# Kernel tuning notes

Measured on AMD Instinct MI355X. Metric: run time of the kernel, lower is better.

The kernel has to match this reference:

```python
import jax, jax.numpy as jnp
import numpy as np
from jax import lax

DIM = 128          # embedding dim
LG = 3             # layer_gnn
LC = 3             # layer_cnn
LO = 2             # layer_output
WIN = 11           # window -> conv kernel 23x23, padding 11 (SAME)
NF = 10000         # n_fingerprint
NW = 10000         # n_word
NA = 4096          # n_atoms
NWORDS = 16384     # protein length


def setup_inputs() -> dict:
    key = jax.random.key(0)
    ks = jax.random.split(key, 16)
    s = 1.0 / np.sqrt(DIM)
    s2 = 1.0 / np.sqrt(2 * DIM)
    K = 2 * WIN + 1
    return {
        "fingerprints": jax.random.randint(ks[0], (NA,), 0, NF),
        # sparse-ish binary adjacency like a molecular graph, scaled up
        "adjacency": (jax.random.uniform(ks[1], (NA, NA)) < 0.005).astype(jnp.float32),
        "words": jax.random.randint(ks[2], (NWORDS,), 0, NW),
        "emb_fp": jax.random.normal(ks[3], (NF, DIM), dtype=jnp.float32) * 0.1,
        "emb_word": jax.random.normal(ks[4], (NW, DIM), dtype=jnp.float32) * 0.1,
        "W_gnn_w": jax.random.normal(ks[5], (LG, DIM, DIM), dtype=jnp.float32) * s,
        "W_gnn_b": jax.random.normal(ks[6], (LG, DIM), dtype=jnp.float32) * s,
        "conv_w": jax.random.normal(ks[7], (LC, 1, 1, K, K), dtype=jnp.float32) * 0.02,
        "conv_b": jax.random.normal(ks[8], (LC, 1), dtype=jnp.float32) * 0.02,
        "W_att_w": jax.random.normal(ks[9], (DIM, DIM), dtype=jnp.float32) * s,
        "W_att_b": jax.random.normal(ks[10], (DIM,), dtype=jnp.float32) * s,
        "W_out_w": jax.random.normal(ks[11], (LO, 2 * DIM, 2 * DIM), dtype=jnp.float32) * s2,
        "W_out_b": jax.random.normal(ks[12], (LO, 2 * DIM), dtype=jnp.float32) * s2,
        "W_int_w": jax.random.normal(ks[13], (1, 2 * DIM), dtype=jnp.float32) * s2,
        "W_int_b": jax.random.normal(ks[14], (1,), dtype=jnp.float32) * s2,
    }


def _linear(x, w, b):
    # torch nn.Linear: y = x @ w.T + b
    return x @ w.T + b


def reference(fingerprints, adjacency, words, emb_fp, emb_word,
              W_gnn_w, W_gnn_b, conv_w, conv_b, W_att_w, W_att_b,
              W_out_w, W_out_b, W_int_w, W_int_b):
    # ---- Compound vector with GNN ----
    xs = emb_fp[fingerprints]                      # [NA, DIM]
    for l in range(LG):
        hs = jax.nn.relu(_linear(xs, W_gnn_w[l], W_gnn_b[l]))
        xs = xs + adjacency @ hs                   # residual message passing
    compound = jnp.mean(xs, axis=0, keepdims=True) # [1, DIM]

    # ---- Protein vector with attention-CNN ----
    ws = emb_word[words]                           # [NWORDS, DIM]
    img = ws[None, None]                           # [1, 1, NWORDS, DIM]
    for l in range(LC):
        img = lax.conv_general_dilated(
            img, conv_w[l], window_strides=(1, 1), padding='SAME',
            dimension_numbers=('NCHW', 'OIHW', 'NCHW'))
        img = img + conv_b[l].reshape(1, -1, 1, 1)
        img = jax.nn.leaky_relu(img, negative_slope=0.01)
    ws = img[0, 0]                                 # [NWORDS, DIM]

    h = jax.nn.relu(_linear(compound, W_att_w, W_att_b))   # [1, DIM]
    hs = jax.nn.relu(_linear(ws, W_att_w, W_att_b))        # [NWORDS, DIM]
    weights = jnp.tanh(h @ hs.T)                            # [1, NWORDS]
    ys = weights.T * hs                                     # [NWORDS, DIM]
    protein = jnp.mean(ys, axis=0, keepdims=True)           # [1, DIM]

    # ---- Concatenate and output ----
    cat = jnp.concatenate((compound, protein), axis=1)      # [1, 2*DIM]
    for l in range(LO):
        cat = jax.nn.relu(_linear(cat, W_out_w[l], W_out_b[l]))
    interaction = _linear(cat, W_int_w, W_int_b)            # [1, 1]
    return interaction
```

## Files before the change

### kernel.cpp

```cpp
#include <hip/hip_runtime.h>

#define DIM 128
#define NA 4096
#define NWORDS 16384
#define MAXNZ 256
#define KW 23
#define PAD 11

__global__ void k_gather(float* __restrict__ out, const float* __restrict__ tab,
                         const int* __restrict__ idx) {
  int t = blockIdx.x * blockDim.x + threadIdx.x;
  int r = t >> 5, c = t & 31;
  ((float4*)out)[t] = ((const float4*)(tab + (size_t)idx[r] * DIM))[c];
}

__global__ void k_adj_scan(int* __restrict__ cnt, int* __restrict__ colx,
                           float* __restrict__ valx, const float* __restrict__ adj) {
  int w = threadIdx.x >> 6, lane = threadIdx.x & 63;
  int row = blockIdx.x * 4 + w;
  const float4* ar = (const float4*)(adj + (size_t)row * NA);
  int count = 0;
  unsigned long long ltm = (1ull << lane) - 1ull;
  for (int c4 = lane; c4 < NA / 4; c4 += 64) {
    float4 v = ar[c4];
    #pragma unroll
    for (int e = 0; e < 4; ++e) {
      float ve = e == 0 ? v.x : e == 1 ? v.y : e == 2 ? v.z : v.w;
      unsigned long long m = __ballot(ve != 0.0f);
      if (ve != 0.0f) {
        int off = count + (int)__popcll(m & ltm);
        if (off < MAXNZ) { colx[row * MAXNZ + off] = c4 * 4 + e; valx[row * MAXNZ + off] = ve; }
      }
      count += (int)__popcll(m);
    }
  }
  if (lane == 0) cnt[row] = count;
}

__global__ __launch_bounds__(256) void k_linear_relu(
    float* __restrict__ out, const float* __restrict__ A,
    const float* __restrict__ W, const float* __restrict__ bias) {
  __shared__ float As[64 * 132];
  __shared__ float Ws[64 * 132];
  int mt = blockIdx.x >> 1, nt = blockIdx.x & 1;
  int r0 = mt * 64, c0 = nt * 64;
  int tid = threadIdx.x;
  for (int q = tid; q < 64 * 32; q += 256) {
    int row = q >> 5, c4 = q & 31;
    *(float4*)&As[row * 132 + c4 * 4] = *(const float4*)&A[(size_t)(r0 + row) * DIM + c4 * 4];
    *(float4*)&Ws[row * 132 + c4 * 4] = *(const float4*)&W[(size_t)(c0 + row) * DIM + c4 * 4];
  }
  __syncthreads();
  int rgr = tid & 15, cgr = tid >> 4;
  float acc[4][4] = {};
  #pragma unroll 4
  for (int k4 = 0; k4 < 32; ++k4) {
    int kk = ((k4 + rgr) & 31) * 4;
    float4 a[4], w[4];
    #pragma unroll
    for (int i = 0; i < 4; ++i) a[i] = *(const float4*)&As[(rgr * 4 + i) * 132 + kk];
    #pragma unroll
    for (int j = 0; j < 4; ++j) w[j] = *(const float4*)&Ws[(cgr * 4 + j) * 132 + kk];
    #pragma unroll
    for (int i = 0; i < 4; ++i)
      #pragma unroll
      for (int j = 0; j < 4; ++j)
        acc[i][j] += a[i].x * w[j].x + a[i].y * w[j].y + a[i].z * w[j].z + a[i].w * w[j].w;
  }
  #pragma unroll
  for (int i = 0; i < 4; ++i) {
    int r = r0 + rgr * 4 + i;
    int c = c0 + cgr * 4;
    float4 bv = *(const float4*)&bias[c];
    float4 o;
    o.x = acc[i][0] + bv.x; o.y = acc[i][1] + bv.y;
    o.z = acc[i][2] + bv.z; o.w = acc[i][3] + bv.w;
    o.x = o.x > 0.f ? o.x : 0.f; o.y = o.y > 0.f ? o.y : 0.f;
    o.z = o.z > 0.f ? o.z : 0.f; o.w = o.w > 0.f ? o.w : 0.f;
    *(float4*)&out[(size_t)r * DIM + c] = o;
  }
}

__global__ void k_spmm(float* __restrict__ xs, const float* __restrict__ hs,
                       const int* __restrict__ cnt, const int* __restrict__ colx,
                       const float* __restrict__ valx, const float* __restrict__ adj) {
  __shared__ int scol[MAXNZ];
  __shared__ float sval[MAXNZ];
  int r = blockIdx.x, d = threadIdx.x;
  int n = cnt[r];
  int m = (n <= MAXNZ) ? n : 0;
  for (int i = d; i < m; i += 128) {
    scol[i] = colx[r * MAXNZ + i];
    sval[i] = valx[r * MAXNZ + i];
  }
  __syncthreads();
  float acc = xs[(size_t)r * DIM + d];
  if (n <= MAXNZ) {
    for (int i = 0; i < n; ++i)
      acc += sval[i] * hs[(size_t)scol[i] * DIM + d];
  } else {
    for (int c = 0; c < NA; ++c) {
      float a = adj[(size_t)r * NA + c];
      if (a != 0.f) acc += a * hs[(size_t)c * DIM + d];
    }
  }
  xs[(size_t)r * DIM + d] = acc;
}

__global__ void k_mean(float* __restrict__ out, const float* __restrict__ in,
                       int rows_per_block, float scale) {
  __shared__ float red[256];
  int d = threadIdx.x & 127, half = threadIdx.x >> 7;
  int r0 = blockIdx.x * rows_per_block;
  float acc = 0.f;
  for (int r = r0 + half; r < r0 + rows_per_block; r += 2)
    acc += in[(size_t)r * DIM + d];
  red[threadIdx.x] = acc;
  __syncthreads();
  if (half == 0) atomicAdd(&out[d], (acc + red[threadIdx.x + 128]) * scale);
}

#define CROWS 16
#define TROWS 38
#define TCOLS 150
#define TSTRT 44
__global__ __launch_bounds__(256, 4) void k_conv(
    float* __restrict__ out, const float* __restrict__ in,
    const float* __restrict__ cw, const float* __restrict__ cb) {
  __shared__ float tileT[TCOLS * TSTRT];
  int r0 = blockIdx.x * CROWS;
  int tid = threadIdx.x;
  for (int p = tid; p < TROWS * TCOLS; p += 256) {
    int rr = p / TCOLS, cc = p - rr * TCOLS;
    int gr = r0 - PAD + rr, gc = cc - PAD;
    float v = 0.f;
    if ((unsigned)gr < NWORDS && (unsigned)gc < DIM) v = in[(size_t)gr * DIM + gc];
    tileT[cc * TSTRT + rr] = v;
  }
  __syncthreads();
  int col = tid & 127, rb = tid >> 7;
  int rbase = rb * 8;
  float acc[8] = {};
  for (int dx = 0; dx < KW; ++dx) {
    const float* src = &tileT[(col + dx) * TSTRT + rbase];
    float4 v4[8];
    #pragma unroll
    for (int q = 0; q < 8; ++q) v4[q] = *(const float4*)&src[q * 4];
    const float* v = (const float*)v4;
    const float* wp = cw + dx;
    #pragma unroll
    for (int dy = 0; dy < KW; ++dy) {
      float wv = wp[dy * KW];
      #pragma unroll
      for (int i = 0; i < 8; ++i) acc[i] += wv * v[i + dy];
    }
  }
  float bias = cb[0];
  #pragma unroll
  for (int i = 0; i < 8; ++i) {
    float x = acc[i] + bias;
    out[(size_t)(r0 + rbase + i) * DIM + col] = x > 0.f ? x : 0.01f * x;
  }
}

__global__ __launch_bounds__(256) void k_attprot(
    float* __restrict__ prot, const float* __restrict__ hsA,
    const float* __restrict__ comp, const float* __restrict__ W,
    const float* __restrict__ b) {
  __shared__ float cvec[DIM];
  __shared__ float hv_s[DIM];
  __shared__ float lw[32];
  __shared__ float red[256];
  int tid = threadIdx.x;
  int w = tid >> 6, lane = tid & 63;
  if (tid < 128) cvec[tid] = comp[tid];
  __syncthreads();
  if (tid < 128) {
    float acc = b[tid];
    #pragma unroll
    for (int k4 = 0; k4 < 32; ++k4) {
      float4 w4 = *(const float4*)&W[tid * DIM + k4 * 4];
      acc += cvec[k4*4+0] * w4.x + cvec[k4*4+1] * w4.y + cvec[k4*4+2] * w4.z + cvec[k4*4+3] * w4.w;
    }
    hv_s[tid] = acc > 0.f ? acc : 0.f;
  }
  __syncthreads();
  int r0 = blockIdx.x * 32;
  float2 hv = ((const float2*)hv_s)[lane];
  for (int rr = w; rr < 32; rr += 4) {
    float2 xv = ((const float2*)(hsA + (size_t)(r0 + rr) * DIM))[lane];
    float dt = hv.x * xv.x + hv.y * xv.y;
    for (int o = 32; o > 0; o >>= 1) dt += __shfl_xor(dt, o);
    if (lane == 0) lw[rr] = tanhf(dt);
  }
  __syncthreads();
  int d = tid & 127, half = tid >> 7;
  float acc = 0.f;
  for (int rr = half; rr < 32; rr += 2)
    acc += lw[rr] * hsA[(size_t)(r0 + rr) * DIM + d];
  red[tid] = acc;
  __syncthreads();
  if (half == 0) atomicAdd(&prot[d], (acc + red[tid + 128]) * (1.f / NWORDS));
}

__global__ __launch_bounds__(256) void k_final(
    float* __restrict__ out, const float* __restrict__ comp, const float* __restrict__ prot,
    const float* __restrict__ Wo, const float* __restrict__ bo,
    const float* __restrict__ Wi, const float* __restrict__ bi) {
  __shared__ float cat[256];
  __shared__ float wred[4];
  int t = threadIdx.x;
  int w = t >> 6, lane = t & 63;
  cat[t] = t < 128 ? comp[t] : prot[t - 128];
  __syncthreads();
  for (int l = 0; l < 2; ++l) {
    const float* Wl = Wo + l * 256 * 256;
    float acc = bo[l * 256 + t];
    #pragma unroll 8
    for (int k4 = 0; k4 < 64; ++k4) {
      float4 w4 = *(const float4*)&Wl[t * 256 + k4 * 4];
      acc += cat[k4*4+0] * w4.x + cat[k4*4+1] * w4.y + cat[k4*4+2] * w4.z + cat[k4*4+3] * w4.w;
    }
    __syncthreads();
    cat[t] = acc > 0.f ? acc : 0.f;
    __syncthreads();
  }
  float r = cat[t] * Wi[t];
  for (int o = 32; o > 0; o >>= 1) r += __shfl_xor(r, o);
  if (lane == 0) wred[w] = r;
  __syncthreads();
  if (t == 0) out[0] = wred[0] + wred[1] + wred[2] + wred[3] + bi[0];
}

extern "C" void kernel_launch(void* const* d_in, const int* in_sizes, int n_in,
                              void* d_out, int out_size, void* d_ws, size_t ws_size,
                              hipStream_t stream) {
  const int*   fingerprints = (const int*)d_in[0];
  const float* adjacency    = (const float*)d_in[1];
  const int*   words        = (const int*)d_in[2];
  const float* emb_fp       = (const float*)d_in[3];
  const float* emb_word     = (const float*)d_in[4];
  const float* W_gnn_w      = (const float*)d_in[5];
  const float* W_gnn_b      = (const float*)d_in[6];
  const float* conv_w       = (const float*)d_in[7];
  const float* conv_b       = (const float*)d_in[8];
  const float* W_att_w      = (const float*)d_in[9];
  const float* W_att_b      = (const float*)d_in[10];
  const float* W_out_w      = (const float*)d_in[11];
  const float* W_out_b      = (const float*)d_in[12];
  const float* W_int_w      = (const float*)d_in[13];
  const float* W_int_b      = (const float*)d_in[14];
  float* out = (float*)d_out;

  float* xs   = (float*)d_ws;
  float* hsb  = xs   + 524288;
  float* valx = hsb  + 524288;
  float* pa   = valx + 1048576;
  float* pb   = pa   + 2097152;
  float* hsA  = pb   + 2097152;
  float* attw = hsA  + 2097152;
  float* small= attw + 16384;
  int*   colx = (int*)(small + 512);
  int*   cntv = colx + 1048576;
  float* comp = small, *prot = small + 128;
  (void)attw;

  hipMemsetAsync(small, 0, 512 * sizeof(float), stream);

  k_gather<<<512, 256, 0, stream>>>(xs, emb_fp, fingerprints);
  k_adj_scan<<<1024, 256, 0, stream>>>(cntv, colx, valx, adjacency);
  for (int l = 0; l < 3; ++l) {
    k_linear_relu<<<128, 256, 0, stream>>>(hsb, xs, W_gnn_w + l * DIM * DIM, W_gnn_b + l * DIM);
    k_spmm<<<NA, 128, 0, stream>>>(xs, hsb, cntv, colx, valx, adjacency);
  }
  k_mean<<<128, 256, 0, stream>>>(comp, xs, 32, 1.0f / NA);

  k_gather<<<2048, 256, 0, stream>>>(pa, emb_word, words);
  k_conv<<<1024, 256, 0, stream>>>(pb, pa, conv_w + 0 * 529, conv_b + 0);
  k_conv<<<1024, 256, 0, stream>>>(pa, pb, conv_w + 1 * 529, conv_b + 1);
  k_conv<<<1024, 256, 0, stream>>>(pb, pa, conv_w + 2 * 529, conv_b + 2);

  k_linear_relu<<<512, 256, 0, stream>>>(hsA, pb, W_att_w, W_att_b);
  k_attprot<<<512, 256, 0, stream>>>(prot, hsA, comp, W_att_w, W_att_b);

  k_final<<<1, 256, 0, stream>>>(out, comp, prot, W_out_w, W_out_b, W_int_w, W_int_b);
}
```

Before: 389.8 us.

## Fuse embedding gathers into adjacency scan and first conv; retune conv LDS reads

Removes both standalone gather kernels. The fingerprint embedding gather moves into the adjacency-scan kernel, and the word embedding gather is folded into the first conv layer's tile load through a template flag. This saves two launches and one 8MB intermediate write and read. The conv inner loop now uses float2 shared-memory reads, a padded stride of 42 instead of 44, and scalar accumulators with explicit FMA. The stride change may alter LDS bank conflicts, and the gathered tile load does scattered reads of the embedding table.

```diff
diff --git a/kernel.cpp b/kernel.cpp
--- a/kernel.cpp
+++ b/kernel.cpp
@@ -7,17 +7,17 @@
 #define KW 23
 #define PAD 11
 
-__global__ void k_gather(float* __restrict__ out, const float* __restrict__ tab,
-                         const int* __restrict__ idx) {
-  int t = blockIdx.x * blockDim.x + threadIdx.x;
-  int r = t >> 5, c = t & 31;
-  ((float4*)out)[t] = ((const float4*)(tab + (size_t)idx[r] * DIM))[c];
-}
-
 __global__ void k_adj_scan(int* __restrict__ cnt, int* __restrict__ colx,
-                           float* __restrict__ valx, const float* __restrict__ adj) {
+                           float* __restrict__ valx, const float* __restrict__ adj,
+                           float* __restrict__ xs, const float* __restrict__ emb_fp,
+                           const int* __restrict__ fingerprints) {
   int w = threadIdx.x >> 6, lane = threadIdx.x & 63;
   int row = blockIdx.x * 4 + w;
+  if (threadIdx.x < 128) {
+    int rr = blockIdx.x * 4 + (threadIdx.x >> 5), c4 = threadIdx.x & 31;
+    ((float4*)(xs + (size_t)rr * DIM))[c4] =
+        ((const float4*)(emb_fp + (size_t)fingerprints[rr] * DIM))[c4];
+  }
   const float4* ar = (const float4*)(adj + (size_t)row * NA);
   int count = 0;
   unsigned long long ltm = (1ull << lane) - 1ull;
@@ -123,9 +123,11 @@
 #define CROWS 16
 #define TROWS 38
 #define TCOLS 150
-#define TSTRT 44
+#define TSTRT 42
+template<int GATHER>
 __global__ __launch_bounds__(256, 4) void k_conv(
     float* __restrict__ out, const float* __restrict__ in,
+    const int* __restrict__ words, const float* __restrict__ emb,
     const float* __restrict__ cw, const float* __restrict__ cb) {
   __shared__ float tileT[TCOLS * TSTRT];
   int r0 = blockIdx.x * CROWS;
@@ -134,33 +136,50 @@
     int rr = p / TCOLS, cc = p - rr * TCOLS;
     int gr = r0 - PAD + rr, gc = cc - PAD;
     float v = 0.f;
-    if ((unsigned)gr < NWORDS && (unsigned)gc < DIM) v = in[(size_t)gr * DIM + gc];
+    if ((unsigned)gr < NWORDS && (unsigned)gc < DIM) {
+      if (GATHER) v = emb[(size_t)words[gr] * DIM + gc];
+      else        v = in[(size_t)gr * DIM + gc];
+    }
     tileT[cc * TSTRT + rr] = v;
   }
   __syncthreads();
   int col = tid & 127, rb = tid >> 7;
   int rbase = rb * 8;
-  float acc[8] = {};
+  float acc0 = 0.f, acc1 = 0.f, acc2 = 0.f, acc3 = 0.f;
+  float acc4 = 0.f, acc5 = 0.f, acc6 = 0.f, acc7 = 0.f;
   for (int dx = 0; dx < KW; ++dx) {
-    const float* src = &tileT[(col + dx) * TSTRT + rbase];
-    float4 v4[8];
-    #pragma unroll
-    for (int q = 0; q < 8; ++q) v4[q] = *(const float4*)&src[q * 4];
-    const float* v = (const float*)v4;
+    float v[30];
+    const float2* src = (const float2*)&tileT[(col + dx) * TSTRT + rbase];
+    #pragma unroll
+    for (int q = 0; q < 15; ++q) {
+      float2 t_ = src[q];
+      v[q * 2 + 0] = t_.x; v[q * 2 + 1] = t_.y;
+    }
     const float* wp = cw + dx;
     #pragma unroll
     for (int dy = 0; dy < KW; ++dy) {
       float wv = wp[dy * KW];
-      #pragma unroll
-      for (int i = 0; i < 8; ++i) acc[i] += wv * v[i + dy];
+      acc0 = __builtin_fmaf(wv, v[dy + 0], acc0);
+      acc1 = __builtin_fmaf(wv, v[dy + 1], acc1);
+      acc2 = __builtin_fmaf(wv, v[dy + 2], acc2);
+      acc3 = __builtin_fmaf(wv, v[dy + 3], acc3);
+      acc4 = __builtin_fmaf(wv, v[dy + 4], acc4);
+      acc5 = __builtin_fmaf(wv, v[dy + 5], acc5);
+      acc6 = __builtin_fmaf(wv, v[dy + 6], acc6);
+      acc7 = __builtin_fmaf(wv, v[dy + 7], acc7);
     }
   }
   float bias = cb[0];
-  #pragma unroll
-  for (int i = 0; i < 8; ++i) {
-    float x = acc[i] + bias;
-    out[(size_t)(r0 + rbase + i) * DIM + col] = x > 0.f ? x : 0.01f * x;
-  }
+  size_t ob = (size_t)(r0 + rbase) * DIM + col;
+  float x;
+  x = acc0 + bias; out[ob + 0 * DIM] = x > 0.f ? x : 0.01f * x;
+  x = acc1 + bias; out[ob + 1 * DIM] = x > 0.f ? x : 0.01f * x;
+  x = acc2 + bias; out[ob + 2 * DIM] = x > 0.f ? x : 0.01f * x;
+  x = acc3 + bias; out[ob + 3 * DIM] = x > 0.f ? x : 0.01f * x;
+  x = acc4 + bias; out[ob + 4 * DIM] = x > 0.f ? x : 0.01f * x;
+  x = acc5 + bias; out[ob + 5 * DIM] = x > 0.f ? x : 0.01f * x;
+  x = acc6 + bias; out[ob + 6 * DIM] = x > 0.f ? x : 0.01f * x;
+  x = acc7 + bias; out[ob + 7 * DIM] = x > 0.f ? x : 0.01f * x;
 }
 
 __global__ __launch_bounds__(256) void k_attprot(
@@ -267,18 +286,16 @@
 
   hipMemsetAsync(small, 0, 512 * sizeof(float), stream);
 
-  k_gather<<<512, 256, 0, stream>>>(xs, emb_fp, fingerprints);
-  k_adj_scan<<<1024, 256, 0, stream>>>(cntv, colx, valx, adjacency);
+  k_adj_scan<<<1024, 256, 0, stream>>>(cntv, colx, valx, adjacency, xs, emb_fp, fingerprints);
   for (int l = 0; l < 3; ++l) {
     k_linear_relu<<<128, 256, 0, stream>>>(hsb, xs, W_gnn_w + l * DIM * DIM, W_gnn_b + l * DIM);
     k_spmm<<<NA, 128, 0, stream>>>(xs, hsb, cntv, colx, valx, adjacency);
   }
   k_mean<<<128, 256, 0, stream>>>(comp, xs, 32, 1.0f / NA);
 
-  k_gather<<<2048, 256, 0, stream>>>(pa, emb_word, words);
-  k_conv<<<1024, 256, 0, stream>>>(pb, pa, conv_w + 0 * 529, conv_b + 0);
-  k_conv<<<1024, 256, 0, stream>>>(pa, pb, conv_w + 1 * 529, conv_b + 1);
-  k_conv<<<1024, 256, 0, stream>>>(pb, pa, conv_w + 2 * 529, conv_b + 2);
+  k_conv<1><<<1024, 256, 0, stream>>>(pb, nullptr, words, emb_word, conv_w + 0 * 529, conv_b + 0);
+  k_conv<0><<<1024, 256, 0, stream>>>(pa, pb, nullptr, nullptr, conv_w + 1 * 529, conv_b + 1);
+  k_conv<0><<<1024, 256, 0, stream>>>(pb, pa, nullptr, nullptr, conv_w + 2 * 529, conv_b + 2);
 
   k_linear_relu<<<512, 256, 0, stream>>>(hsA, pb, W_att_w, W_att_b);
   k_attprot<<<512, 256, 0, stream>>>(prot, hsA, comp, W_att_w, W_att_b);
```

Measured after the change: 363.8 us. 1.07x faster.
